# Kernel tuning notes

Measured on AMD Instinct MI355X. Metric: run time of the kernel, lower is better.

Reference implementation:

```python
import jax, jax.numpy as jnp
import numpy as np

H = 200  # hardcoded utterance_size == hidden_size in the module


def _lstm(Wih, Whh, bih, bhh, xs, h0, c0):
    """Run a torch-style LSTM (gate order i,f,g,o) over xs: [T,H] -> final hidden [H]."""
    b = bih + bhh
    def cell(carry, x):
        h, c = carry
        g = x @ Wih.T + h @ Whh.T + b
        i, f, gg, o = jnp.split(g, 4, axis=-1)
        c = jax.nn.sigmoid(f) * c + jax.nn.sigmoid(i) * jnp.tanh(gg)
        h = jax.nn.sigmoid(o) * jnp.tanh(c)
        return (h, c), None
    (h, _), _ = jax.lax.scan(cell, (h0, c0), xs)
    return h


def setup_inputs() -> dict:
    key = jax.random.key(0)
    S, W = 255, 512  # sentences (odd, so middle exists), words per sentence
    ks = jax.random.split(key, 24)
    d = {}
    d["utterances"] = jax.random.normal(ks[0], (S, W, H), jnp.float32)
    d["h0_sent"] = jax.random.normal(ks[1], (S, H), jnp.float32)  # per-sentence random h0 (torch.randn in original)
    d["h0_prev"] = jax.random.normal(ks[2], (H,), jnp.float32)
    d["h0_post"] = jax.random.normal(ks[3], (H,), jnp.float32)
    idx = 4
    for name in ["ctx", "main", "prev", "post"]:
        d[name + "_Wih"] = jax.random.normal(ks[idx], (4 * H, H), jnp.float32) * 0.05; idx += 1
        d[name + "_Whh"] = jax.random.normal(ks[idx], (4 * H, H), jnp.float32) * 0.05; idx += 1
        d[name + "_bih"] = jax.random.normal(ks[idx], (4 * H,), jnp.float32) * 0.05; idx += 1
        d[name + "_bhh"] = jax.random.normal(ks[idx], (4 * H,), jnp.float32) * 0.05; idx += 1
    d["fc_W"] = jax.random.normal(ks[idx], (H, 2 * H), jnp.float32) * 0.05
    d["fc_b"] = jnp.zeros((H,), jnp.float32)
    return d


def reference(utterances, h0_sent, h0_prev, h0_post,
              ctx_Wih, ctx_Whh, ctx_bih, ctx_bhh,
              main_Wih, main_Whh, main_bih, main_bhh,
              prev_Wih, prev_Whh, prev_bih, prev_bhh,
              post_Wih, post_Whh, post_bih, post_bhh,
              fc_W, fc_b):
    S = utterances.shape[0]
    mid = (S - 1) // 2
    z = jnp.zeros((H,), utterances.dtype)  # c0 = 0 for every LSTM
    # Context LSTM over every sentence (vectorized over sentences), word-level recurrence via scan.
    ctx_final = jax.vmap(
        lambda xs, h0: _lstm(ctx_Wih, ctx_Whh, ctx_bih, ctx_bhh, xs, h0, z)
    )(utterances, h0_sent)  # [S, H]
    # Middle sentence uses main_lstm instead.
    main_final = _lstm(main_Wih, main_Whh, main_bih, main_bhh,
                       utterances[mid], h0_sent[mid], z)  # [H]
    sent_emb = ctx_final.at[mid].set(main_final)  # [S, H]
    # prev_lstm runs over sentence embeddings 0..mid; prev_out = output at the middle step.
    prev_out = _lstm(prev_Wih, prev_Whh, prev_bih, prev_bhh,
                     sent_emb[:mid + 1], h0_prev, z)  # [H]
    # post_lstm runs reversed S-1..mid; post_out = output at the middle step.
    post_out = _lstm(post_Wih, post_Whh, post_bih, post_bhh,
                     sent_emb[mid:][::-1], h0_post, z)  # [H]
    feat = jnp.concatenate([prev_out, post_out])  # [2H]
    return feat @ fc_W.T + fc_b  # [H]
```

## Files before the change

### kernel.cpp

```cpp
#include <hip/hip_runtime.h>
#include <hip/hip_fp16.h>
#include <cstdint>

typedef _Float16 f16;
typedef _Float16 f16x2 __attribute__((ext_vector_type(2)));
typedef _Float16 f16x4 __attribute__((ext_vector_type(4)));
typedef _Float16 f16x8 __attribute__((ext_vector_type(8)));
typedef float f32x4 __attribute__((ext_vector_type(4)));

#define kH 200
#define kG 800
#define kS 255
#define kW 512
#define kMid 127

#define OFF_WF   209715200ULL
#define OFF_BS   212275200ULL
#define OFF_SENT 212288000ULL
#define OFF_XPP  212492032ULL
#define OFF_OUTS 212901632ULL

__device__ __forceinline__ float sigf(float x) { return 1.0f / (1.0f + __expf(-x)); }
__device__ __forceinline__ float tanhf_(float x) { return 1.0f - 2.0f / (__expf(2.0f * x) + 1.0f); }

__global__ __launch_bounds__(256) void ABHUE_prep(
    const float* W0, const float* W1, const float* W2, const float* W3,
    const float* W4, const float* W5, const float* W6, const float* W7,
    const float* B0i, const float* B0h, const float* B1i, const float* B1h,
    const float* B2i, const float* B2h, const float* B3i, const float* B3h,
    f16* wdst, float* bdst)
{
  int idx = blockIdx.x * 256 + threadIdx.x;
  const int WN = kG * kH;
  if (idx < 8 * WN) {
    int m = idx / WN, off = idx % WN;
    const float* src = m == 0 ? W0 : m == 1 ? W1 : m == 2 ? W2 : m == 3 ? W3
                     : m == 4 ? W4 : m == 5 ? W5 : m == 6 ? W6 : W7;
    int np = off / kH, k = off - np * kH;
    int u = np >> 2, g = np & 3;
    wdst[idx] = (f16)src[(size_t)(g * kH + u) * kH + k];
  } else {
    int j = idx - 8 * WN;
    if (j < 4 * kG) {
      int st = j / kG, np = j - st * kG;
      int u = np >> 2, g = np & 3;
      int n = g * kH + u;
      const float* bi = st == 0 ? B0i : st == 1 ? B1i : st == 2 ? B2i : B3i;
      const float* bh = st == 0 ? B0h : st == 1 ? B1h : st == 2 ? B2h : B3h;
      bdst[j] = bi[n] + bh[n];
    }
  }
}

#define BM 64
#define BKP 232
__global__ __launch_bounds__(256) void ABHUE_gemm_x(
    const float* __restrict__ A, const f16* __restrict__ Wf,
    const float* __restrict__ bias, f16* __restrict__ X, int rev)
{
  __shared__ __align__(16) f16 Al[BM * BKP];
  __shared__ __align__(16) f16 Bl[BM * BKP];
  int tid = threadIdx.x;
  int m0 = blockIdx.x * BM;

  #pragma unroll
  for (int it = 0; it < 4; ++it) {
    int idx = tid + 256 * it;
    int row = idx >> 4, dw = idx & 15;
    *(uint32_t*)(&Al[row * BKP + 200 + dw * 2]) = 0u;
    *(uint32_t*)(&Bl[row * BKP + 200 + dw * 2]) = 0u;
  }
  for (int it = 0; it < 13; ++it) {
    int q = tid + 256 * it;
    if (q < 3200) {
      int row = q / 50, c = q % 50;
      int rg = m0 + row; if (rev >= 0) rg = rev - rg;
      const float4 v = *(const float4*)(A + (size_t)rg * kH + c * 4);
      f16x2 p0; p0[0] = (f16)v.x; p0[1] = (f16)v.y;
      f16x2 p1; p1[0] = (f16)v.z; p1[1] = (f16)v.w;
      uint2 pk; pk.x = __builtin_bit_cast(uint32_t, p0); pk.y = __builtin_bit_cast(uint32_t, p1);
      *(uint2*)(&Al[row * BKP + c * 4]) = pk;
    }
  }
  int wv = tid >> 6, lane = tid & 63;
  int lr = lane & 15, lq = lane >> 4;

  for (int nt = 0; nt < 13; ++nt) {
    int n0 = nt * 64;
    __syncthreads();
    for (int it = 0; it < 7; ++it) {
      int q = tid + 256 * it;
      if (q < 1600) {
        int row = q / 25, c = q % 25;
        int ng = n0 + row;
        uint4 v = (ng < kG) ? *(const uint4*)(Wf + (size_t)ng * kH + c * 8)
                            : make_uint4(0, 0, 0, 0);
        *(uint4*)(&Bl[row * BKP + c * 8]) = v;
      }
    }
    __syncthreads();
    f32x4 acc0 = {0,0,0,0}, acc1 = {0,0,0,0}, acc2 = {0,0,0,0}, acc3 = {0,0,0,0};
    #pragma unroll
    for (int ks = 0; ks < 7; ++ks) {
      int k0 = ks * 32 + lq * 8;
      f16x8 a  = *(const f16x8*)(&Al[(wv * 16 + lr) * BKP + k0]);
      f16x8 b0 = *(const f16x8*)(&Bl[( 0 + lr) * BKP + k0]);
      f16x8 b1 = *(const f16x8*)(&Bl[(16 + lr) * BKP + k0]);
      f16x8 b2 = *(const f16x8*)(&Bl[(32 + lr) * BKP + k0]);
      f16x8 b3 = *(const f16x8*)(&Bl[(48 + lr) * BKP + k0]);
      acc0 = __builtin_amdgcn_mfma_f32_16x16x32_f16(a, b0, acc0, 0, 0, 0);
      acc1 = __builtin_amdgcn_mfma_f32_16x16x32_f16(a, b1, acc1, 0, 0, 0);
      acc2 = __builtin_amdgcn_mfma_f32_16x16x32_f16(a, b2, acc2, 0, 0, 0);
      acc3 = __builtin_amdgcn_mfma_f32_16x16x32_f16(a, b3, acc3, 0, 0, 0);
    }
    auto epi = [&](f32x4 acc, int nn) {
      int col = n0 + nn * 16 + lr;
      if (col < kG) {
        float bv = bias[col];
        #pragma unroll
        for (int rr = 0; rr < 4; ++rr) {
          int m = m0 + wv * 16 + lq * 4 + rr;
          X[(size_t)m * kG + col] = (f16)(acc[rr] + bv);
        }
      }
    };
    epi(acc0, 0); epi(acc1, 1); epi(acc2, 2); epi(acc3, 3);
  }
}

static __device__ void lstm_m1(const f16* __restrict__ X, const f16* __restrict__ Whh,
                               const float* __restrict__ h0, int nsteps,
                               float* __restrict__ out)
{
  __shared__ __align__(16) f16 hbuf[2][224];
  __shared__ __align__(16) float gsh[kG];
  int tid = threadIdx.x;
  int lane = tid & 63, wv = tid >> 6;
  int lr = lane & 15, lq = lane >> 4;
  int t0 = (50 * wv) >> 3;
  int cnt = ((50 * (wv + 1)) >> 3) - t0;

  f16x8 bf[7][7];
  #pragma unroll
  for (int i = 0; i < 7; ++i) {
    if (i < cnt) {
      int n = (t0 + i) * 16 + lr;
      const f16* wrow = Whh + (size_t)n * kH;
      #pragma unroll
      for (int kt = 0; kt < 6; ++kt)
        bf[i][kt] = *(const f16x8*)(wrow + kt * 32 + lq * 8);
      bf[i][6] = (lq == 0) ? *(const f16x8*)(wrow + 192)
                           : (f16x8){0,0,0,0,0,0,0,0};
    }
  }

  int ul = 4 * t0 + lane;
  bool cellp = (lane < 4 * cnt);

  if (tid < 24) { hbuf[0][200 + tid] = (f16)0; hbuf[1][200 + tid] = (f16)0; }
  if (cellp) hbuf[0][ul] = (f16)h0[ul];
  float cst = 0.f, hout = 0.f;
  uint2 xc = make_uint2(0, 0);
  if (cellp) xc = *(const uint2*)(X + 4 * ul);
  __syncthreads();

  for (int t = 0; t < nsteps; ++t) {
    const f16* hb = hbuf[t & 1];
    uint2 xn = make_uint2(0, 0);
    if (cellp && t + 1 < nsteps)
      xn = *(const uint2*)(X + (size_t)(t + 1) * kG + 4 * ul);

    f16x8 af[7];
    #pragma unroll
    for (int kt = 0; kt < 7; ++kt)
      af[kt] = *(const f16x8*)(hb + kt * 32 + lq * 8);

    #pragma unroll
    for (int ip = 0; ip < 3; ++ip) {
      f32x4 a0 = {0.f,0.f,0.f,0.f}, a1 = {0.f,0.f,0.f,0.f};
      #pragma unroll
      for (int kt = 0; kt < 7; ++kt) {
        a0 = __builtin_amdgcn_mfma_f32_16x16x32_f16(af[kt], bf[2*ip][kt], a0, 0, 0, 0);
        a1 = __builtin_amdgcn_mfma_f32_16x16x32_f16(af[kt], bf[2*ip+1][kt], a1, 0, 0, 0);
      }
      if (lq == 0) {
        gsh[(t0 + 2*ip) * 16 + lr]     = a0[0];
        gsh[(t0 + 2*ip + 1) * 16 + lr] = a1[0];
      }
    }
    if (cnt == 7) {
      f32x4 a0 = {0.f,0.f,0.f,0.f};
      #pragma unroll
      for (int kt = 0; kt < 7; ++kt)
        a0 = __builtin_amdgcn_mfma_f32_16x16x32_f16(af[kt], bf[6][kt], a0, 0, 0, 0);
      if (lq == 0) gsh[(t0 + 6) * 16 + lr] = a0[0];
    }

    asm volatile("s_waitcnt lgkmcnt(0)" ::: "memory");

    if (cellp) {
      float4 gv = *(const float4*)(gsh + 4 * ul);
      f16x4 xv = __builtin_bit_cast(f16x4, xc);
      float gi = gv.x + (float)xv[0];
      float gf = gv.y + (float)xv[1];
      float gg = gv.z + (float)xv[2];
      float go = gv.w + (float)xv[3];
      cst  = sigf(gf) * cst + sigf(gi) * tanhf_(gg);
      hout = sigf(go) * tanhf_(cst);
      hbuf[(t & 1) ^ 1][ul] = (f16)hout;
    }
    xc = xn;
    __syncthreads();
  }
  if (out != nullptr && cellp) out[ul] = hout;
}

__global__ __launch_bounds__(512, 2) void ABHUE_lstm_batch(
    const f16* __restrict__ Xall, const f16* __restrict__ Wctx, const f16* __restrict__ Wmain,
    const float* __restrict__ h0s, float* __restrict__ sent)
{
  int s = blockIdx.x;
  const f16* X = Xall + (size_t)s * kW * kG;
  const f16* Wh = (s == 255) ? Wmain : Wctx;
  int hrow = (s == 255) ? kMid : s;
  const float* h0 = h0s + (size_t)hrow * kH;
  float* out = (s == kMid) ? nullptr : sent + (size_t)hrow * kH;
  lstm_m1(X, Wh, h0, kW, out);
}

__global__ __launch_bounds__(512, 2) void ABHUE_lstm_pp(
    const f16* __restrict__ Xpp, const f16* __restrict__ Wprev, const f16* __restrict__ Wpost,
    const float* __restrict__ h0prev, const float* __restrict__ h0post, float* __restrict__ outs)
{
  int s = blockIdx.x;
  lstm_m1(Xpp + (size_t)s * 128 * kG, s ? Wpost : Wprev, s ? h0post : h0prev, 128,
          outs + (size_t)s * kH);
}

__global__ __launch_bounds__(256) void ABHUE_fc(
    const float* __restrict__ feat, const float* __restrict__ fcW,
    const float* __restrict__ fcb, float* __restrict__ outp)
{
  __shared__ float fs[2 * kH];
  int tid = threadIdx.x;
  for (int i = tid; i < 2 * kH; i += 256) fs[i] = feat[i];
  __syncthreads();
  if (tid < kH) {
    float acc = fcb[tid];
    #pragma unroll 4
    for (int j = 0; j < 2 * kH; ++j) acc = fmaf(fcW[tid * 2 * kH + j], fs[j], acc);
    outp[tid] = acc;
  }
}

extern "C" void kernel_launch(void* const* d_in, const int* in_sizes, int n_in,
                              void* d_out, int out_size, void* d_ws, size_t ws_size,
                              hipStream_t stream) {
  const float* utt    = (const float*)d_in[0];
  const float* h0s    = (const float*)d_in[1];
  const float* h0prev = (const float*)d_in[2];
  const float* h0post = (const float*)d_in[3];
  const float* wih[4] = {(const float*)d_in[4],  (const float*)d_in[8],
                         (const float*)d_in[12], (const float*)d_in[16]};
  const float* whh[4] = {(const float*)d_in[5],  (const float*)d_in[9],
                         (const float*)d_in[13], (const float*)d_in[17]};
  const float* bih[4] = {(const float*)d_in[6],  (const float*)d_in[10],
                         (const float*)d_in[14], (const float*)d_in[18]};
  const float* bhh[4] = {(const float*)d_in[7],  (const float*)d_in[11],
                         (const float*)d_in[15], (const float*)d_in[19]};
  const float* fcW = (const float*)d_in[20];
  const float* fcb = (const float*)d_in[21];

  char* base  = (char*)d_ws;
  f16*   Xall = (f16*)base;
  f16*   Wf   = (f16*)(base + OFF_WF);
  float* bsum = (float*)(base + OFF_BS);
  float* sent = (float*)(base + OFF_SENT);
  f16*   Xpp  = (f16*)(base + OFF_XPP);
  float* outs = (float*)(base + OFF_OUTS);

  const int WN = kG * kH;
  ABHUE_prep<<<(8 * WN + 4 * kG + 255) / 256, 256, 0, stream>>>(
      wih[0], whh[0], wih[1], whh[1], wih[2], whh[2], wih[3], whh[3],
      bih[0], bhh[0], bih[1], bhh[1], bih[2], bhh[2], bih[3], bhh[3],
      Wf, bsum);

  ABHUE_gemm_x<<<2040, 256, 0, stream>>>(utt, Wf + 0 * WN, bsum + 0, Xall, -1);
  ABHUE_gemm_x<<<8, 256, 0, stream>>>(utt + (size_t)kMid * kW * kH, Wf + 2 * WN,
                                      bsum + 800, Xall + (size_t)255 * kW * kG, -1);
  ABHUE_lstm_batch<<<256, 512, 0, stream>>>(Xall, Wf + 1 * WN, Wf + 3 * WN, h0s, sent);
  ABHUE_gemm_x<<<2, 256, 0, stream>>>(sent, Wf + 4 * WN, bsum + 1600, Xpp, -1);
  ABHUE_gemm_x<<<2, 256, 0, stream>>>(sent, Wf + 6 * WN, bsum + 2400, Xpp + (size_t)128 * kG, 254);
  ABHUE_lstm_pp<<<2, 512, 0, stream>>>(Xpp, Wf + 5 * WN, Wf + 7 * WN, h0prev, h0post, outs);
  ABHUE_fc<<<1, 256, 0, stream>>>(outs, fcW, fcb, (float*)d_out);
}
```

Before: 1.309 ms.

## Split LSTM cell update into two phases overlapping remaining gate MFMAs

Reorders each timestep so the first four gate tiles of a wave are computed and written to shared memory first. Lanes 0-15 then run their cell update while the last two or three MFMA tiles are still in flight; the remaining lanes update once those tiles land. Only lanes with lr==0 load the hidden-state A fragments, since only MFMA row 0 is consumed, which cuts LDS reads. Tile ranges per wave are also assigned explicitly. The aim is to shorten the serial critical path of each recurrence step. The cost is more code and an extra LDS wait.

```diff
diff --git a/kernel.cpp b/kernel.cpp
--- a/kernel.cpp
+++ b/kernel.cpp
@@ -137,8 +137,8 @@
   int tid = threadIdx.x;
   int lane = tid & 63, wv = tid >> 6;
   int lr = lane & 15, lq = lane >> 4;
-  int t0 = (50 * wv) >> 3;
-  int cnt = ((50 * (wv + 1)) >> 3) - t0;
+  int cnt = (wv == 3 || wv == 4) ? 7 : 6;
+  int t0 = 6 * wv + (wv > 3) + (wv > 4);
 
   f16x8 bf[7][7];
   #pragma unroll
@@ -162,43 +162,58 @@
   float cst = 0.f, hout = 0.f;
   uint2 xc = make_uint2(0, 0);
   if (cellp) xc = *(const uint2*)(X + 4 * ul);
+
+  f16x8 af[7];
+  #pragma unroll
+  for (int kt = 0; kt < 7; ++kt) af[kt] = (f16x8){0,0,0,0,0,0,0,0};
   __syncthreads();
 
   for (int t = 0; t < nsteps; ++t) {
     const f16* hb = hbuf[t & 1];
+    f16* hn = hbuf[(t & 1) ^ 1];
     uint2 xn = make_uint2(0, 0);
     if (cellp && t + 1 < nsteps)
       xn = *(const uint2*)(X + (size_t)(t + 1) * kG + 4 * ul);
 
-    f16x8 af[7];
+    if (lr == 0) {
+      #pragma unroll
+      for (int kt = 0; kt < 7; ++kt)
+        af[kt] = *(const f16x8*)(hb + kt * 32 + lq * 8);
+    }
+
+    {
+      f32x4 a0 = {0.f,0.f,0.f,0.f}, a1 = {0.f,0.f,0.f,0.f};
+      #pragma unroll
+      for (int kt = 0; kt < 7; ++kt) {
+        a0 = __builtin_amdgcn_mfma_f32_16x16x32_f16(af[kt], bf[0][kt], a0, 0, 0, 0);
+        a1 = __builtin_amdgcn_mfma_f32_16x16x32_f16(af[kt], bf[1][kt], a1, 0, 0, 0);
+      }
+      if (lq == 0) { gsh[(t0 + 0) * 16 + lr] = a0[0]; gsh[(t0 + 1) * 16 + lr] = a1[0]; }
+    }
+    {
+      f32x4 a0 = {0.f,0.f,0.f,0.f}, a1 = {0.f,0.f,0.f,0.f};
+      #pragma unroll
+      for (int kt = 0; kt < 7; ++kt) {
+        a0 = __builtin_amdgcn_mfma_f32_16x16x32_f16(af[kt], bf[2][kt], a0, 0, 0, 0);
+        a1 = __builtin_amdgcn_mfma_f32_16x16x32_f16(af[kt], bf[3][kt], a1, 0, 0, 0);
+      }
+      if (lq == 0) { gsh[(t0 + 2) * 16 + lr] = a0[0]; gsh[(t0 + 3) * 16 + lr] = a1[0]; }
+    }
+
+    f32x4 b0 = {0.f,0.f,0.f,0.f}, b1 = {0.f,0.f,0.f,0.f}, b2 = {0.f,0.f,0.f,0.f};
     #pragma unroll
-    for (int kt = 0; kt < 7; ++kt)
-      af[kt] = *(const f16x8*)(hb + kt * 32 + lq * 8);
-
-    #pragma unroll
-    for (int ip = 0; ip < 3; ++ip) {
-      f32x4 a0 = {0.f,0.f,0.f,0.f}, a1 = {0.f,0.f,0.f,0.f};
-      #pragma unroll
-      for (int kt = 0; kt < 7; ++kt) {
-        a0 = __builtin_amdgcn_mfma_f32_16x16x32_f16(af[kt], bf[2*ip][kt], a0, 0, 0, 0);
-        a1 = __builtin_amdgcn_mfma_f32_16x16x32_f16(af[kt], bf[2*ip+1][kt], a1, 0, 0, 0);
-      }
-      if (lq == 0) {
-        gsh[(t0 + 2*ip) * 16 + lr]     = a0[0];
-        gsh[(t0 + 2*ip + 1) * 16 + lr] = a1[0];
-      }
+    for (int kt = 0; kt < 7; ++kt) {
+      b0 = __builtin_amdgcn_mfma_f32_16x16x32_f16(af[kt], bf[4][kt], b0, 0, 0, 0);
+      b1 = __builtin_amdgcn_mfma_f32_16x16x32_f16(af[kt], bf[5][kt], b1, 0, 0, 0);
     }
     if (cnt == 7) {
-      f32x4 a0 = {0.f,0.f,0.f,0.f};
       #pragma unroll
       for (int kt = 0; kt < 7; ++kt)
-        a0 = __builtin_amdgcn_mfma_f32_16x16x32_f16(af[kt], bf[6][kt], a0, 0, 0, 0);
-      if (lq == 0) gsh[(t0 + 6) * 16 + lr] = a0[0];
+        b2 = __builtin_amdgcn_mfma_f32_16x16x32_f16(af[kt], bf[6][kt], b2, 0, 0, 0);
     }
 
     asm volatile("s_waitcnt lgkmcnt(0)" ::: "memory");
-
-    if (cellp) {
+    if (lane < 16) {
       float4 gv = *(const float4*)(gsh + 4 * ul);
       f16x4 xv = __builtin_bit_cast(f16x4, xc);
       float gi = gv.x + (float)xv[0];
@@ -207,7 +222,25 @@
       float go = gv.w + (float)xv[3];
       cst  = sigf(gf) * cst + sigf(gi) * tanhf_(gg);
       hout = sigf(go) * tanhf_(cst);
-      hbuf[(t & 1) ^ 1][ul] = (f16)hout;
+      hn[ul] = (f16)hout;
+    }
+
+    if (lq == 0) {
+      gsh[(t0 + 4) * 16 + lr] = b0[0];
+      gsh[(t0 + 5) * 16 + lr] = b1[0];
+      if (cnt == 7) gsh[(t0 + 6) * 16 + lr] = b2[0];
+    }
+    asm volatile("s_waitcnt lgkmcnt(0)" ::: "memory");
+    if (lane >= 16 && cellp) {
+      float4 gv = *(const float4*)(gsh + 4 * ul);
+      f16x4 xv = __builtin_bit_cast(f16x4, xc);
+      float gi = gv.x + (float)xv[0];
+      float gf = gv.y + (float)xv[1];
+      float gg = gv.z + (float)xv[2];
+      float go = gv.w + (float)xv[3];
+      cst  = sigf(gf) * cst + sigf(gi) * tanhf_(gg);
+      hout = sigf(go) * tanhf_(cst);
+      hn[ul] = (f16)hout;
     }
     xc = xn;
     __syncthreads();
```

Result: slower. 1.438 ms (+9.8%).
